# Optimization experiments

Measured on AMD Instinct MI355X. Metric: run time of the kernel, lower is better.

The kernel has to match this reference:

```python
import jax, jax.numpy as jnp
import numpy as np

EMBED = 1024
HEADS = 16
HEAD_DIM = EMBED // HEADS
BATCH = 8
SEQ = 2048


def setup_inputs() -> dict:
    key = jax.random.key(0)
    ks = jax.random.split(key, 6)
    s = EMBED ** -0.5
    x = jax.random.normal(ks[0], (BATCH, SEQ, EMBED), dtype=jnp.float32)
    # weights stored as (in, out); applied as x @ W (equivalent to torch Linear with W.T)
    Wq = jax.random.normal(ks[1], (EMBED, EMBED), dtype=jnp.float32) * s
    Wk = jax.random.normal(ks[2], (EMBED, EMBED), dtype=jnp.float32) * s
    Wv = jax.random.normal(ks[3], (EMBED, EMBED), dtype=jnp.float32) * s
    Wo = jax.random.normal(ks[4], (EMBED, EMBED), dtype=jnp.float32) * s
    bo = jax.random.normal(ks[5], (EMBED,), dtype=jnp.float32) * 0.01
    return {"x": x, "Wq": Wq, "Wk": Wk, "Wv": Wv, "Wo": Wo, "bo": bo}


def reference(x, Wq, Wk, Wv, Wo, bo):
    N, S, E = x.shape
    H, D = HEADS, HEAD_DIM
    # project and reshape to (N, H, S, D) exactly as the torch code (view + permute)
    q = (x @ Wq).reshape(N, S, H, D).transpose(0, 2, 1, 3)
    k = (x @ Wk).reshape(N, S, H, D).transpose(0, 2, 1, 3)
    v = (x @ Wv).reshape(N, S, H, D).transpose(0, 2, 1, 3)
    # Faithful to source: einsum subscripts applied to ALREADY-PERMUTED tensors,
    # so 'a'/'b' range over heads and 's' over seq -> energy is (N, H, H).
    energy = jnp.einsum('nasd,nbsd->nab', q, k)
    attention = jax.nn.softmax(energy / np.sqrt(D).astype(np.float32), axis=2)
    # second einsum: sum over key-heads (b) and value-heads (h) independently
    out = jnp.einsum('nab,nhsd->nasd', attention, v)  # (N, H, S, D)
    out = out.transpose(0, 2, 1, 3).reshape(N, S, E)
    return out @ Wo + bo
```

## Files before the change

### kernel.cpp

```cpp
#include <hip/hip_runtime.h>
#include <hip/hip_bf16.h>


typedef _Float16 half8 __attribute__((ext_vector_type(8)));
typedef float f32x4 __attribute__((ext_vector_type(4)));

__device__ __forceinline__ half8 cvt8(float4 a, float4 b) {
  half8 h;
  h[0] = (_Float16)a.x; h[1] = (_Float16)a.y;
  h[2] = (_Float16)a.z; h[3] = (_Float16)a.w;
  h[4] = (_Float16)b.x; h[5] = (_Float16)b.y;
  h[6] = (_Float16)b.z; h[7] = (_Float16)b.w;
  return h;
}

__global__ __launch_bounds__(256) void prep(const float* __restrict__ Wv,
                                            const float* __restrict__ Wo,
                                            _Float16* __restrict__ BvF,
                                            _Float16* __restrict__ BoF) {
  const int b = blockIdx.x, t = threadIdx.x;
  const int l = t & 63, lr = l & 15, lk = (l >> 4) << 3;
  if (b < 32) {
    const int s = b, ctg = t >> 6;
    const int d = (ctg << 4) + lr;
    const int k0 = (s << 5) + lk;
    float sum[8] = {};
#pragma unroll
    for (int h = 0; h < 16; ++h)
#pragma unroll
      for (int j = 0; j < 8; ++j)
        sum[j] += Wv[(k0 + j) * 1024 + h * 64 + d];
    half8 hv;
#pragma unroll
    for (int j = 0; j < 8; ++j) hv[j] = (_Float16)sum[j];
    ((half8*)BvF)[(s * 4 + ctg) * 64 + l] = hv;
  } else {
    const int g = b - 32;
    const int kk = t >> 7, jh = (t >> 6) & 1;
    const int e = (g << 4) + lr;
    const int kb = (kk << 5) + lk + (jh << 2);
    float sum[4] = {};
#pragma unroll
    for (int h = 0; h < 16; ++h)
#pragma unroll
      for (int j = 0; j < 4; ++j)
        sum[j] += Wo[(h * 64 + kb + j) * 1024 + e];
    _Float16 hv[4];
#pragma unroll
    for (int j = 0; j < 4; ++j) hv[j] = (_Float16)sum[j];
    *(uint2*)&BoF[(((g * 2 + kk) * 64 + l) << 3) + (jh << 2)] =
        *(const uint2*)hv;
  }
}

__global__ __launch_bounds__(256) void fused(const float* __restrict__ x,
                                             const _Float16* __restrict__ BvF,
                                             const _Float16* __restrict__ BoF,
                                             const float* __restrict__ bo,
                                             float* __restrict__ out) {
  __shared__ float red[4][16][64];
  __shared__ __align__(16) _Float16 Af[16][72];
  const int t = threadIdx.x, q = t >> 6, l = t & 63;
  const int lr = l & 15, lk8 = (l >> 4) << 3;
  const int r0 = (int)blockIdx.x << 4;

  {
    const float* xp = &x[(r0 + lr) * 1024 + (q << 8) + lk8];
    const half8* bp = (const half8*)BvF;
    f32x4 acc[4] = {};
    float4 xv[2][2];
    half8 br[2][4];
    xv[0][0] = *(const float4*)(xp);
    xv[0][1] = *(const float4*)(xp + 4);
#pragma unroll
    for (int ct = 0; ct < 4; ++ct)
      br[0][ct] = bp[((q * 8) * 4 + ct) * 64 + l];
#pragma unroll
    for (int kc = 0; kc < 8; ++kc) {
      const int cur = kc & 1;
      if (kc + 1 < 8) {
        const float* xq = xp + (kc + 1) * 32;
        xv[cur ^ 1][0] = *(const float4*)(xq);
        xv[cur ^ 1][1] = *(const float4*)(xq + 4);
#pragma unroll
        for (int ct = 0; ct < 4; ++ct)
          br[cur ^ 1][ct] = bp[((q * 8 + kc + 1) * 4 + ct) * 64 + l];
      }
      const half8 ah = cvt8(xv[cur][0], xv[cur][1]);
#pragma unroll
      for (int ct = 0; ct < 4; ++ct)
        acc[ct] = __builtin_amdgcn_mfma_f32_16x16x32_f16(ah, br[cur][ct], acc[ct], 0, 0, 0);
    }
#pragma unroll
    for (int ct = 0; ct < 4; ++ct)
#pragma unroll
      for (int j = 0; j < 4; ++j)
        red[q][((l >> 4) << 2) + j][(ct << 4) + lr] = acc[ct][j];
  }
  __syncthreads();
  {
    const int row = t >> 4, c4 = (t & 15) << 2;
    float4 s0 = *(const float4*)&red[0][row][c4];
    const float4 s1 = *(const float4*)&red[1][row][c4];
    const float4 s2 = *(const float4*)&red[2][row][c4];
    const float4 s3 = *(const float4*)&red[3][row][c4];
    _Float16 hv[4];
    hv[0] = (_Float16)(s0.x + s1.x + s2.x + s3.x);
    hv[1] = (_Float16)(s0.y + s1.y + s2.y + s3.y);
    hv[2] = (_Float16)(s0.z + s1.z + s2.z + s3.z);
    hv[3] = (_Float16)(s0.w + s1.w + s2.w + s3.w);
    *(uint2*)&Af[row][c4] = *(const uint2*)hv;
  }
  __syncthreads();
  {
    half8 afr[2];
#pragma unroll
    for (int kk = 0; kk < 2; ++kk)
      afr[kk] = *(const half8*)&Af[lr][kk * 32 + lk8];
    const half8* bp = (const half8*)BoF;
    const int g0 = q << 4;
    half8 brg[2][2];
    float bvr[2];
#pragma unroll
    for (int kk = 0; kk < 2; ++kk)
      brg[0][kk] = bp[(g0 * 2 + kk) * 64 + l];
    bvr[0] = bo[(g0 << 4) + lr];
#pragma unroll
    for (int g = 0; g < 16; ++g) {
      const int cur = g & 1;
      if (g + 1 < 16) {
#pragma unroll
        for (int kk = 0; kk < 2; ++kk)
          brg[cur ^ 1][kk] = bp[((g0 + g + 1) * 2 + kk) * 64 + l];
        bvr[cur ^ 1] = bo[((g0 + g + 1) << 4) + lr];
      }
      f32x4 a = {};
#pragma unroll
      for (int kk = 0; kk < 2; ++kk)
        a = __builtin_amdgcn_mfma_f32_16x16x32_f16(afr[kk], brg[cur][kk], a, 0, 0, 0);
      const int col = (q << 8) + (g << 4) + lr;
      const float bv = bvr[cur];
#pragma unroll
      for (int j = 0; j < 4; ++j)
        out[(r0 + ((l >> 4) << 2) + j) * 1024 + col] = a[j] + bv;
    }
  }
}

extern "C" void kernel_launch(void* const* d_in, const int* in_sizes, int n_in,
                              void* d_out, int out_size, void* d_ws, size_t ws_size,
                              hipStream_t stream) {
  const float* x = (const float*)d_in[0];
  const float* Wv = (const float*)d_in[3];
  const float* Wo = (const float*)d_in[4];
  const float* bo = (const float*)d_in[5];
  float* out = (float*)d_out;

  _Float16* BvF = (_Float16*)d_ws;
  _Float16* BoF = BvF + 65536;

  prep<<<96, 256, 0, stream>>>(Wv, Wo, BvF, BoF);
  fused<<<1024, 256, 0, stream>>>(x, BvF, BoF, bo, out);
}
```

Baseline: 152.2 us.

## Use 8 waves per block, split K finer, store output as float4 via swapped MFMA

Doubles the block to 512 threads so each wave handles 128 of the 1024 input columns instead of 256, giving more in-flight memory loads per block for the memory-bound read of x. The reduction across waves now sums eight partials. The output GEMM swaps its MFMA operands so each lane holds four consecutive columns, which allows float4 stores of the result and float4 bias loads. The software prefetch of the B fragments is removed in the first stage, and the shared reduction buffer doubles, which may reduce occupancy.

```diff
diff --git a/kernel.cpp b/kernel.cpp
--- a/kernel.cpp
+++ b/kernel.cpp
@@ -53,96 +53,90 @@
   }
 }
 
-__global__ __launch_bounds__(256) void fused(const float* __restrict__ x,
-                                             const _Float16* __restrict__ BvF,
-                                             const _Float16* __restrict__ BoF,
-                                             const float* __restrict__ bo,
-                                             float* __restrict__ out) {
-  __shared__ float red[4][16][64];
+__global__ __launch_bounds__(512, 8) void fused(const float* __restrict__ x,
+                                                const _Float16* __restrict__ BvF,
+                                                const _Float16* __restrict__ BoF,
+                                                const float* __restrict__ bo,
+                                                float* __restrict__ out) {
+  __shared__ float red[8][16][64];
   __shared__ __align__(16) _Float16 Af[16][72];
-  const int t = threadIdx.x, q = t >> 6, l = t & 63;
+  const int t = threadIdx.x, w = t >> 6, l = t & 63;
   const int lr = l & 15, lk8 = (l >> 4) << 3;
   const int r0 = (int)blockIdx.x << 4;
 
   {
-    const float* xp = &x[(r0 + lr) * 1024 + (q << 8) + lk8];
+    const float* xp = &x[(r0 + lr) * 1024 + (w << 7) + lk8];
     const half8* bp = (const half8*)BvF;
     f32x4 acc[4] = {};
     float4 xv[2][2];
-    half8 br[2][4];
     xv[0][0] = *(const float4*)(xp);
     xv[0][1] = *(const float4*)(xp + 4);
 #pragma unroll
-    for (int ct = 0; ct < 4; ++ct)
-      br[0][ct] = bp[((q * 8) * 4 + ct) * 64 + l];
-#pragma unroll
-    for (int kc = 0; kc < 8; ++kc) {
+    for (int kc = 0; kc < 4; ++kc) {
       const int cur = kc & 1;
-      if (kc + 1 < 8) {
+      if (kc + 1 < 4) {
         const float* xq = xp + (kc + 1) * 32;
         xv[cur ^ 1][0] = *(const float4*)(xq);
         xv[cur ^ 1][1] = *(const float4*)(xq + 4);
+      }
+      half8 br[4];
 #pragma unroll
-        for (int ct = 0; ct < 4; ++ct)
-          br[cur ^ 1][ct] = bp[((q * 8 + kc + 1) * 4 + ct) * 64 + l];
-      }
+      for (int ct = 0; ct < 4; ++ct)
+        br[ct] = bp[((w * 4 + kc) * 4 + ct) * 64 + l];
       const half8 ah = cvt8(xv[cur][0], xv[cur][1]);
 #pragma unroll
       for (int ct = 0; ct < 4; ++ct)
-        acc[ct] = __builtin_amdgcn_mfma_f32_16x16x32_f16(ah, br[cur][ct], acc[ct], 0, 0, 0);
+        acc[ct] = __builtin_amdgcn_mfma_f32_16x16x32_f16(ah, br[ct], acc[ct], 0, 0, 0);
     }
 #pragma unroll
     for (int ct = 0; ct < 4; ++ct)
 #pragma unroll
       for (int j = 0; j < 4; ++j)
-        red[q][((l >> 4) << 2) + j][(ct << 4) + lr] = acc[ct][j];
+        red[w][((l >> 4) << 2) + j][(ct << 4) + lr] = acc[ct][j];
   }
   __syncthreads();
   {
-    const int row = t >> 4, c4 = (t & 15) << 2;
-    float4 s0 = *(const float4*)&red[0][row][c4];
-    const float4 s1 = *(const float4*)&red[1][row][c4];
-    const float4 s2 = *(const float4*)&red[2][row][c4];
-    const float4 s3 = *(const float4*)&red[3][row][c4];
-    _Float16 hv[4];
-    hv[0] = (_Float16)(s0.x + s1.x + s2.x + s3.x);
-    hv[1] = (_Float16)(s0.y + s1.y + s2.y + s3.y);
-    hv[2] = (_Float16)(s0.z + s1.z + s2.z + s3.z);
-    hv[3] = (_Float16)(s0.w + s1.w + s2.w + s3.w);
-    *(uint2*)&Af[row][c4] = *(const uint2*)hv;
+    const int row = t >> 5, c = (t & 31) << 1;
+    float sx = 0.f, sy = 0.f;
+#pragma unroll
+    for (int p = 0; p < 8; ++p) {
+      float2 v = *(const float2*)&red[p][row][c];
+      sx += v.x; sy += v.y;
+    }
+    _Float16 hv[2] = {(_Float16)sx, (_Float16)sy};
+    *(unsigned int*)&Af[row][c] = *(const unsigned int*)hv;
   }
   __syncthreads();
   {
-    half8 afr[2];
+    half8 tfr[2];
 #pragma unroll
     for (int kk = 0; kk < 2; ++kk)
-      afr[kk] = *(const half8*)&Af[lr][kk * 32 + lk8];
+      tfr[kk] = *(const half8*)&Af[lr][kk * 32 + lk8];
     const half8* bp = (const half8*)BoF;
-    const int g0 = q << 4;
-    half8 brg[2][2];
-    float bvr[2];
+    const int g0 = w << 3;
+    half8 wfr[2][2];
+    float4 bvr[2];
 #pragma unroll
     for (int kk = 0; kk < 2; ++kk)
-      brg[0][kk] = bp[(g0 * 2 + kk) * 64 + l];
-    bvr[0] = bo[(g0 << 4) + lr];
+      wfr[0][kk] = bp[(g0 * 2 + kk) * 64 + l];
+    bvr[0] = *(const float4*)&bo[(g0 << 4) + ((l >> 4) << 2)];
 #pragma unroll
-    for (int g = 0; g < 16; ++g) {
+    for (int g = 0; g < 8; ++g) {
       const int cur = g & 1;
-      if (g + 1 < 16) {
+      if (g + 1 < 8) {
 #pragma unroll
         for (int kk = 0; kk < 2; ++kk)
-          brg[cur ^ 1][kk] = bp[((g0 + g + 1) * 2 + kk) * 64 + l];
-        bvr[cur ^ 1] = bo[((g0 + g + 1) << 4) + lr];
+          wfr[cur ^ 1][kk] = bp[((g0 + g + 1) * 2 + kk) * 64 + l];
+        bvr[cur ^ 1] = *(const float4*)&bo[((g0 + g + 1) << 4) + ((l >> 4) << 2)];
       }
       f32x4 a = {};
 #pragma unroll
       for (int kk = 0; kk < 2; ++kk)
-        a = __builtin_amdgcn_mfma_f32_16x16x32_f16(afr[kk], brg[cur][kk], a, 0, 0, 0);
-      const int col = (q << 8) + (g << 4) + lr;
-      const float bv = bvr[cur];
-#pragma unroll
-      for (int j = 0; j < 4; ++j)
-        out[(r0 + ((l >> 4) << 2) + j) * 1024 + col] = a[j] + bv;
+        a = __builtin_amdgcn_mfma_f32_16x16x32_f16(wfr[cur][kk], tfr[kk], a, 0, 0, 0);
+      const int col = ((g0 + g) << 4) + ((l >> 4) << 2);
+      const float4 bv = bvr[cur];
+      float4 o = make_float4(a[0] + bv.x, a[1] + bv.y, a[2] + bv.z, a[3] + bv.w);
+      *(float4*)&out[(r0 + lr) * 1024 + col] = o;
     }
   }
 }
@@ -160,5 +154,5 @@
   _Float16* BoF = BvF + 65536;
 
   prep<<<96, 256, 0, stream>>>(Wv, Wo, BvF, BoF);
-  fused<<<1024, 256, 0, stream>>>(x, BvF, BoF, bo, out);
+  fused<<<1024, 512, 0, stream>>>(x, BvF, BoF, bo, out);
 }
```

Result: slower. 164.1 us (+7.8%).

## Issue all loads upfront with inline asm and stage output through LDS for coalesced stores

Applied to the files above, without the earlier changes.

The first GEMM stage now issues all x and weight loads up front with inline-asm global_load_dwordx4 and explicit vmcnt waits, using a deeper 4-slot weight ring in place of double buffering. The output stage swaps the operands of the MFMA so each lane produces a transposed fragment, writes the tiles to a padded shared buffer in two halves, and then stores rows with coalesced float4 writes plus a vectorized bias add. It also sets launch bounds to 3 blocks per SM. This trades more registers and LDS plus extra barriers for fewer exposed memory latencies and wider, coalesced global stores. Hand-written vmcnt counts are fragile if the compiler inserts other memory ops.

```diff
diff --git a/kernel.cpp b/kernel.cpp
--- a/kernel.cpp
+++ b/kernel.cpp
@@ -4,6 +4,16 @@
 
 typedef _Float16 half8 __attribute__((ext_vector_type(8)));
 typedef float f32x4 __attribute__((ext_vector_type(4)));
+
+#define GLOADO(dst, addr, IMM)                                   \
+  asm volatile("global_load_dwordx4 %0, %1, off offset:" #IMM    \
+               : "=v"(dst) : "v"(addr))
+
+#define WAITVM(N)                                                \
+  do {                                                           \
+    asm volatile("s_waitcnt vmcnt(" #N ")" ::: "memory");        \
+    __builtin_amdgcn_sched_barrier(0);                           \
+  } while (0)
 
 __device__ __forceinline__ half8 cvt8(float4 a, float4 b) {
   half8 h;
@@ -53,57 +63,72 @@
   }
 }
 
-__global__ __launch_bounds__(256) void fused(const float* __restrict__ x,
-                                             const _Float16* __restrict__ BvF,
-                                             const _Float16* __restrict__ BoF,
-                                             const float* __restrict__ bo,
-                                             float* __restrict__ out) {
-  __shared__ float red[4][16][64];
+__global__ __launch_bounds__(256, 3) void fused(const float* __restrict__ x,
+                                                const _Float16* __restrict__ BvF,
+                                                const _Float16* __restrict__ BoF,
+                                                const float* __restrict__ bo,
+                                                float* __restrict__ out) {
+  __shared__ __align__(16) float shbuf[16 * 516];
   __shared__ __align__(16) _Float16 Af[16][72];
   const int t = threadIdx.x, q = t >> 6, l = t & 63;
   const int lr = l & 15, lk8 = (l >> 4) << 3;
   const int r0 = (int)blockIdx.x << 4;
 
   {
-    const float* xp = &x[(r0 + lr) * 1024 + (q << 8) + lk8];
-    const half8* bp = (const half8*)BvF;
+    const char* xb = (const char*)&x[(r0 + lr) * 1024 + (q << 8) + lk8];
+    const char* bvb = (const char*)BvF + (((q * 32) * 64) + l) * 16;
+    float4 xv[16];
+    half8 br[4][4];
     f32x4 acc[4] = {};
-    float4 xv[2][2];
-    half8 br[2][4];
-    xv[0][0] = *(const float4*)(xp);
-    xv[0][1] = *(const float4*)(xp + 4);
+    GLOADO(br[0][0], bvb, 0);    GLOADO(br[0][1], bvb, 1024);
+    GLOADO(br[0][2], bvb, 2048); GLOADO(br[0][3], bvb, 3072);
+    {
+      const char* b1 = bvb + 4096;
+      GLOADO(br[1][0], b1, 0);    GLOADO(br[1][1], b1, 1024);
+      GLOADO(br[1][2], b1, 2048); GLOADO(br[1][3], b1, 3072);
+    }
+    GLOADO(xv[0], xb, 0);     GLOADO(xv[1], xb, 16);
+    GLOADO(xv[2], xb, 128);   GLOADO(xv[3], xb, 144);
+    GLOADO(xv[4], xb, 256);   GLOADO(xv[5], xb, 272);
+    GLOADO(xv[6], xb, 384);   GLOADO(xv[7], xb, 400);
+    GLOADO(xv[8], xb, 512);   GLOADO(xv[9], xb, 528);
+    GLOADO(xv[10], xb, 640);  GLOADO(xv[11], xb, 656);
+    GLOADO(xv[12], xb, 768);  GLOADO(xv[13], xb, 784);
+    GLOADO(xv[14], xb, 896);  GLOADO(xv[15], xb, 912);
+
+#define CHUNK(c, N)                                                            \
+    do {                                                                       \
+      if ((c) + 2 < 8) {                                                       \
+        const char* bk = bvb + ((c) + 2) * 4096;                               \
+        GLOADO(br[((c) + 2) & 3][0], bk, 0);                                   \
+        GLOADO(br[((c) + 2) & 3][1], bk, 1024);                                \
+        GLOADO(br[((c) + 2) & 3][2], bk, 2048);                                \
+        GLOADO(br[((c) + 2) & 3][3], bk, 3072);                                \
+      }                                                                        \
+      WAITVM(N);                                                               \
+      half8 ah = cvt8(xv[2 * (c)], xv[2 * (c) + 1]);                           \
+      acc[0] = __builtin_amdgcn_mfma_f32_16x16x32_f16(ah, br[(c) & 3][0], acc[0], 0, 0, 0); \
+      acc[1] = __builtin_amdgcn_mfma_f32_16x16x32_f16(ah, br[(c) & 3][1], acc[1], 0, 0, 0); \
+      acc[2] = __builtin_amdgcn_mfma_f32_16x16x32_f16(ah, br[(c) & 3][2], acc[2], 0, 0, 0); \
+      acc[3] = __builtin_amdgcn_mfma_f32_16x16x32_f16(ah, br[(c) & 3][3], acc[3], 0, 0, 0); \
+    } while (0)
+
+    CHUNK(0, 18); CHUNK(1, 16); CHUNK(2, 8); CHUNK(3, 8);
+    CHUNK(4, 8);  CHUNK(5, 8);  CHUNK(6, 4); CHUNK(7, 0);
+#undef CHUNK
 #pragma unroll
     for (int ct = 0; ct < 4; ++ct)
-      br[0][ct] = bp[((q * 8) * 4 + ct) * 64 + l];
-#pragma unroll
-    for (int kc = 0; kc < 8; ++kc) {
-      const int cur = kc & 1;
-      if (kc + 1 < 8) {
-        const float* xq = xp + (kc + 1) * 32;
-        xv[cur ^ 1][0] = *(const float4*)(xq);
-        xv[cur ^ 1][1] = *(const float4*)(xq + 4);
-#pragma unroll
-        for (int ct = 0; ct < 4; ++ct)
-          br[cur ^ 1][ct] = bp[((q * 8 + kc + 1) * 4 + ct) * 64 + l];
-      }
-      const half8 ah = cvt8(xv[cur][0], xv[cur][1]);
-#pragma unroll
-      for (int ct = 0; ct < 4; ++ct)
-        acc[ct] = __builtin_amdgcn_mfma_f32_16x16x32_f16(ah, br[cur][ct], acc[ct], 0, 0, 0);
-    }
-#pragma unroll
-    for (int ct = 0; ct < 4; ++ct)
 #pragma unroll
       for (int j = 0; j < 4; ++j)
-        red[q][((l >> 4) << 2) + j][(ct << 4) + lr] = acc[ct][j];
+        shbuf[((q * 16) + (((l >> 4) << 2) + j)) * 64 + (ct << 4) + lr] = acc[ct][j];
   }
   __syncthreads();
   {
     const int row = t >> 4, c4 = (t & 15) << 2;
-    float4 s0 = *(const float4*)&red[0][row][c4];
-    const float4 s1 = *(const float4*)&red[1][row][c4];
-    const float4 s2 = *(const float4*)&red[2][row][c4];
-    const float4 s3 = *(const float4*)&red[3][row][c4];
+    float4 s0 = *(const float4*)&shbuf[(0 * 16 + row) * 64 + c4];
+    const float4 s1 = *(const float4*)&shbuf[(1 * 16 + row) * 64 + c4];
+    const float4 s2 = *(const float4*)&shbuf[(2 * 16 + row) * 64 + c4];
+    const float4 s3 = *(const float4*)&shbuf[(3 * 16 + row) * 64 + c4];
     _Float16 hv[4];
     hv[0] = (_Float16)(s0.x + s1.x + s2.x + s3.x);
     hv[1] = (_Float16)(s0.y + s1.y + s2.y + s3.y);
@@ -112,38 +137,49 @@
     *(uint2*)&Af[row][c4] = *(const uint2*)hv;
   }
   __syncthreads();
-  {
-    half8 afr[2];
-#pragma unroll
-    for (int kk = 0; kk < 2; ++kk)
-      afr[kk] = *(const half8*)&Af[lr][kk * 32 + lk8];
-    const half8* bp = (const half8*)BoF;
-    const int g0 = q << 4;
-    half8 brg[2][2];
-    float bvr[2];
-#pragma unroll
-    for (int kk = 0; kk < 2; ++kk)
-      brg[0][kk] = bp[(g0 * 2 + kk) * 64 + l];
-    bvr[0] = bo[(g0 << 4) + lr];
-#pragma unroll
-    for (int g = 0; g < 16; ++g) {
-      const int cur = g & 1;
-      if (g + 1 < 16) {
-#pragma unroll
-        for (int kk = 0; kk < 2; ++kk)
-          brg[cur ^ 1][kk] = bp[((g0 + g + 1) * 2 + kk) * 64 + l];
-        bvr[cur ^ 1] = bo[((g0 + g + 1) << 4) + lr];
-      }
-      f32x4 a = {};
-#pragma unroll
-      for (int kk = 0; kk < 2; ++kk)
-        a = __builtin_amdgcn_mfma_f32_16x16x32_f16(afr[kk], brg[cur][kk], a, 0, 0, 0);
-      const int col = (q << 8) + (g << 4) + lr;
-      const float bv = bvr[cur];
-#pragma unroll
-      for (int j = 0; j < 4; ++j)
-        out[(r0 + ((l >> 4) << 2) + j) * 1024 + col] = a[j] + bv;
+
+  half8 tfr[2];
+  tfr[0] = *(const half8*)&Af[lr][lk8];
+  tfr[1] = *(const half8*)&Af[lr][32 + lk8];
+  const int wcol = q << 7;
+  const int jj4 = (l >> 4) << 2;
+
+  for (int h = 0; h < 2; ++h) {
+    const char* bob = (const char*)BoF + ((((h * 32 + q * 8) * 2) * 64) + l) * 16;
+    half8 wfr[8][2];
+    GLOADO(wfr[0][0], bob, 0); GLOADO(wfr[0][1], bob, 1024);
+    { const char* a2 = bob + 1 * 2048; GLOADO(wfr[1][0], a2, 0); GLOADO(wfr[1][1], a2, 1024); }
+    { const char* a2 = bob + 2 * 2048; GLOADO(wfr[2][0], a2, 0); GLOADO(wfr[2][1], a2, 1024); }
+    { const char* a2 = bob + 3 * 2048; GLOADO(wfr[3][0], a2, 0); GLOADO(wfr[3][1], a2, 1024); }
+    { const char* a2 = bob + 4 * 2048; GLOADO(wfr[4][0], a2, 0); GLOADO(wfr[4][1], a2, 1024); }
+    { const char* a2 = bob + 5 * 2048; GLOADO(wfr[5][0], a2, 0); GLOADO(wfr[5][1], a2, 1024); }
+    { const char* a2 = bob + 6 * 2048; GLOADO(wfr[6][0], a2, 0); GLOADO(wfr[6][1], a2, 1024); }
+    { const char* a2 = bob + 7 * 2048; GLOADO(wfr[7][0], a2, 0); GLOADO(wfr[7][1], a2, 1024); }
+
+#define PHG(g, N)                                                              \
+    do {                                                                       \
+      WAITVM(N);                                                               \
+      f32x4 a = {};                                                            \
+      a = __builtin_amdgcn_mfma_f32_16x16x32_f16(wfr[g][0], tfr[0], a, 0, 0, 0); \
+      a = __builtin_amdgcn_mfma_f32_16x16x32_f16(wfr[g][1], tfr[1], a, 0, 0, 0); \
+      *(float4*)&shbuf[lr * 516 + wcol + (g) * 16 + jj4] =                     \
+          make_float4(a[0], a[1], a[2], a[3]);                                 \
+    } while (0)
+
+    PHG(0, 14); PHG(1, 12); PHG(2, 10); PHG(3, 8);
+    PHG(4, 6);  PHG(5, 4);  PHG(6, 2);  PHG(7, 0);
+#undef PHG
+    __syncthreads();
+#pragma unroll
+    for (int i = 0; i < 8; ++i) {
+      const int idx = i * 256 + t;
+      const int row = idx >> 7, c4 = (idx & 127) << 2;
+      float4 v = *(const float4*)&shbuf[row * 516 + c4];
+      float4 bb = *(const float4*)&bo[(h << 9) + c4];
+      *(float4*)&out[(r0 + row) * 1024 + (h << 9) + c4] =
+          make_float4(v.x + bb.x, v.y + bb.y, v.z + bb.z, v.w + bb.w);
     }
+    __syncthreads();
   }
 }
 
```

Result: faster. 142.0 us (-6.7%).
